# Performance work log

Hardware: AMD Instinct MI355X
Metric: run time of the kernel (lower is better)

## Reference

```python
import jax, jax.numpy as jnp
import numpy as np

B, L, D_MODEL = 2, 2048, 1024
D_STATE, D_CONV, EXPAND, DT_RANK = 16, 4, 2, 64
D_INNER = EXPAND * D_MODEL


def setup_inputs() -> dict:
    key = jax.random.key(0)
    ks = jax.random.split(key, 12)
    s = 0.02
    A_log = jnp.log(jnp.broadcast_to(jnp.arange(1, D_STATE + 1, dtype=jnp.float32), (D_INNER, D_STATE)))
    return {
        "x": jax.random.normal(ks[0], (B, L, D_MODEL), jnp.float32),
        "W_in": jax.random.normal(ks[1], (2 * D_INNER, D_MODEL), jnp.float32) * s,
        "conv_w": jax.random.normal(ks[2], (D_INNER, 1, D_CONV), jnp.float32) * 0.2,
        "conv_b": jax.random.normal(ks[3], (D_INNER,), jnp.float32) * s,
        "W_xp": jax.random.normal(ks[4], (DT_RANK + 2 * D_STATE, D_INNER), jnp.float32) * s,
        "W_dt": jax.random.normal(ks[5], (D_INNER, DT_RANK), jnp.float32) * 0.1,
        "b_dt": jax.random.uniform(ks[6], (D_INNER,), jnp.float32, -4.6, -2.3),  # ~softplus^-1 of small dt
        "A_log": A_log,
        "D": jnp.ones((D_INNER,), jnp.float32),
        "W_out_ssm": jax.random.normal(ks[7], (D_MODEL, D_INNER), jnp.float32) * s,
        "W_out": jax.random.normal(ks[8], (D_MODEL, D_MODEL), jnp.float32) * s,
        "b_out": jnp.zeros((D_MODEL,), jnp.float32),
    }


def _mamba_block(x, W_in, conv_w, conv_b, W_xp, W_dt, b_dt, A_log, D, W_out_ssm, W_out, b_out):
    d_inner = conv_b.shape[0]
    d_state = A_log.shape[1]
    dt_rank = W_dt.shape[1]
    d_conv = conv_w.shape[-1]

    # in_proj -> x branch and gate z
    xz = x @ W_in.T                         # [B, L, 2*d_inner]
    xin, z = jnp.split(xz, 2, axis=-1)

    # causal depthwise conv over time
    xc = jnp.transpose(xin, (0, 2, 1))      # [B, d_inner, L]
    xc = jax.lax.conv_general_dilated(
        xc, conv_w, window_strides=(1,), padding=[(d_conv - 1, 0)],
        feature_group_count=d_inner)
    xc = jax.nn.silu(xc + conv_b[None, :, None])
    xs = jnp.transpose(xc, (0, 2, 1))       # [B, L, d_inner]

    # input-dependent dt, B, C
    x_dbl = xs @ W_xp.T                     # [B, L, dt_rank + 2*d_state]
    dt, Bm, Cm = jnp.split(x_dbl, [dt_rank, dt_rank + d_state], axis=-1)
    dt = jax.nn.softplus(dt @ W_dt.T + b_dt)  # [B, L, d_inner]

    A = -jnp.exp(A_log)                     # [d_inner, d_state]

    def step(h, inp):
        dt_t, B_t, C_t, x_t = inp           # [B,di] [B,ds] [B,ds] [B,di]
        dA = jnp.exp(dt_t[:, :, None] * A)                      # [B, di, ds]
        h = h * dA + (dt_t * x_t)[:, :, None] * B_t[:, None, :]  # [B, di, ds]
        y = jnp.einsum('bds,bs->bd', h, C_t)
        return h, y

    h0 = jnp.zeros((x.shape[0], d_inner, d_state), x.dtype)
    tm = lambda a: jnp.swapaxes(a, 0, 1)    # time-major
    _, ys = jax.lax.scan(step, h0, (tm(dt), tm(Bm), tm(Cm), tm(xs)))
    y = jnp.swapaxes(ys, 0, 1)              # [B, L, d_inner]

    y = y + xs * D
    y = y * jax.nn.silu(z)
    y = y @ W_out_ssm.T                     # mamba-internal out_proj -> d_model
    return y @ W_out.T + b_out              # wrapper out_proj


def reference(x, W_in, conv_w, conv_b, W_xp, W_dt, b_dt, A_log, D, W_out_ssm, W_out, b_out):
    return _mamba_block(x, W_in, conv_w, conv_b, W_xp, W_dt, b_dt, A_log, D, W_out_ssm, W_out, b_out)
```

## Files before the change

### kernel.cpp

```cpp
#include <hip/hip_runtime.h>
#include <hip/hip_bf16.h>
#include <cmath>
#include <cstdint>

typedef __bf16 bf16_t;
typedef bf16_t bf16x8 __attribute__((ext_vector_type(8)));
typedef bf16_t bf16x4 __attribute__((ext_vector_type(4)));
typedef float f32x4 __attribute__((ext_vector_type(4)));

#define BB 2
#define LL 2048
#define DMODEL 1024
#define DINNER 2048
#define DSTATE 16
#define NC 64
#define CHUNK 32
#define KSEG 256

#define EXP2F(x) __builtin_amdgcn_exp2f(x)

#define CVT_N0 1048576
#define CVT_N1 2097152
#define CVT_N2 2129920
#define CVT_N3 2392064
#define CVT_NB0 9344
#define CVT_NB1 10368
#define CVT_NBT 10880
__global__ __launch_bounds__(256) void k_cvt_all(
    const float* __restrict__ x, const float* __restrict__ Win,
    const float* __restrict__ Wdt, const float* __restrict__ Wo,
    const float* __restrict__ Wxp, const float* __restrict__ Wos,
    bf16_t* __restrict__ x_b, bf16_t* __restrict__ Win_b,
    bf16_t* __restrict__ Wdt_b, bf16_t* __restrict__ Wo_b,
    bf16_t* __restrict__ Wxp_b, bf16_t* __restrict__ WosT_b) {
    const int tid = threadIdx.x;
    if (blockIdx.x < CVT_NB0) {
        int i = blockIdx.x * 256 + tid;
        const float* src; bf16_t* dst; int j;
        if (i < CVT_N0)      { src = x;   dst = x_b;   j = i; }
        else if (i < CVT_N1) { src = Win; dst = Win_b; j = i - CVT_N0; }
        else if (i < CVT_N2) { src = Wdt; dst = Wdt_b; j = i - CVT_N1; }
        else                 { src = Wo;  dst = Wo_b;  j = i - CVT_N2; }
        float4 v = reinterpret_cast<const float4*>(src)[j];
        bf16x4 o;
        o[0] = (bf16_t)v.x; o[1] = (bf16_t)v.y; o[2] = (bf16_t)v.z; o[3] = (bf16_t)v.w;
        reinterpret_cast<bf16x4*>(dst)[j] = o;
    } else if (blockIdx.x < CVT_NB1) {
        int i = (blockIdx.x - CVT_NB0) * 256 + tid;
        int r = i >> 11, c = i & (DINNER - 1);
        float v = (r < 96) ? Wxp[r * DINNER + c] : 0.f;
        Wxp_b[i] = (bf16_t)v;
    } else {
        __shared__ float tile[64][65];
        const int bid = blockIdx.x - CVT_NB1;
        const int m0 = (bid & 15) * 64;
        const int d0 = (bid >> 4) * 64;
        const int dl = tid & 63;
        #pragma unroll 4
        for (int i = 0; i < 16; ++i) {
            const int mr = (tid >> 6) + i * 4;
            tile[dl][mr] = Wos[(size_t)(m0 + mr) * DINNER + d0 + dl];
        }
        __syncthreads();
        const int dr = tid >> 2;
        const int q  = tid & 3;
        bf16_t* op = WosT_b + (size_t)(d0 + dr) * DMODEL + m0 + q * 16;
        bf16x8 v0, v1;
        #pragma unroll
        for (int j = 0; j < 8; ++j) v0[j] = (bf16_t)tile[dr][q * 16 + j];
        #pragma unroll
        for (int j = 0; j < 8; ++j) v1[j] = (bf16_t)tile[dr][q * 16 + 8 + j];
        reinterpret_cast<bf16x8*>(op)[0] = v0;
        reinterpret_cast<bf16x8*>(op)[1] = v1;
    }
}

__device__ __forceinline__ void gload16(const void* g, void* l) {
    __builtin_amdgcn_global_load_lds(
        (const __attribute__((address_space(1))) void*)g,
        (__attribute__((address_space(3))) void*)l,
        16, 0, 0);
}

__global__ __launch_bounds__(256) void k_gemm3(
    const bf16_t* __restrict__ x_b, const bf16_t* __restrict__ Win_b,
    const bf16_t* __restrict__ Wo_b, const bf16_t* __restrict__ WosT_b,
    bf16_t* __restrict__ Wc_b, bf16_t* __restrict__ xin_b,
    bf16_t* __restrict__ zsT) {
    __shared__ bf16_t sA[2][128 * 32];
    __shared__ bf16_t sB[2][128 * 32];
    const int tid = threadIdx.x;
    const int wid = tid >> 6, lane = tid & 63;

    const int bid = (blockIdx.x & 7) * 144 + (blockIdx.x >> 3);
    const bf16_t* A; const bf16_t* Bt; int N, tile, sub;
    if (bid < 128)      { sub = 0; A = Wo_b;  Bt = WosT_b; N = 2048; tile = bid; }
    else if (bid < 640) { sub = 1; A = x_b;   Bt = Win_b;  N = 2048; tile = bid - 128; }
    else                { sub = 2; A = Win_b + (size_t)DINNER * DMODEL; Bt = x_b; N = 4096; tile = bid - 640; }
    const int ntile = N >> 7;
    const int m0 = (tile / ntile) << 7;
    const int n0 = (tile % ntile) << 7;
    const int wr = wid >> 1, wc = wid & 1;
    f32x4 acc[4][4] = {};

    const bf16_t* ap = A + (size_t)(m0 + (tid >> 2)) * 1024 + (tid & 3) * 8;
    const bf16_t* bp = Bt + (size_t)(n0 + (tid >> 2)) * 1024 + (tid & 3) * 8;
    const int lm = lane & 15, lk = (lane >> 4) * 8;

    auto stage = [&](int buf, int kt) {
        char* dA = (char*)sA[buf] + wid * 1024;
        char* dB = (char*)sB[buf] + wid * 1024;
        gload16(ap + kt, dA);
        gload16(ap + kt + (size_t)64 * 1024, dA + 4096);
        gload16(bp + kt, dB);
        gload16(bp + kt + (size_t)64 * 1024, dB + 4096);
    };

    stage(0, 0);
    __syncthreads();
    int cur = 0;
    for (int kt = 0; kt < 1024; kt += 32) {
        if (kt + 32 < 1024) stage(cur ^ 1, kt + 32);
        const bf16_t* rA = sA[cur] + (wr * 64 + lm) * 32 + lk;
        const bf16_t* rB = sB[cur] + (wc * 64 + lm) * 32 + lk;
        bf16x8 fa[4], fb[4];
        #pragma unroll
        for (int i = 0; i < 4; ++i) fa[i] = *(const bf16x8*)(rA + i * 16 * 32);
        #pragma unroll
        for (int j = 0; j < 4; ++j) fb[j] = *(const bf16x8*)(rB + j * 16 * 32);
        __builtin_amdgcn_s_setprio(1);
        #pragma unroll
        for (int i = 0; i < 4; ++i)
            #pragma unroll
            for (int j = 0; j < 4; ++j)
                acc[i][j] = __builtin_amdgcn_mfma_f32_16x16x32_bf16(fa[i], fb[j], acc[i][j], 0, 0, 0);
        __builtin_amdgcn_s_setprio(0);
        __syncthreads();
        cur ^= 1;
    }

    const int row0 = m0 + wr * 64 + (lane >> 4) * 4;
    const int col0 = n0 + wc * 64 + lm;
    #pragma unroll
    for (int i = 0; i < 4; ++i) {
        #pragma unroll
        for (int j = 0; j < 4; ++j) {
            #pragma unroll
            for (int r = 0; r < 4; ++r) {
                int row = row0 + i * 16 + r;
                int c = col0 + j * 16;
                float v = acc[i][j][r];
                if (sub == 0)      Wc_b[(size_t)row * DINNER + c] = (bf16_t)v;
                else if (sub == 1) xin_b[(size_t)row * DINNER + c] = (bf16_t)v;
                else               zsT[(size_t)row * (BB * LL) + c] = (bf16_t)(v / (1.f + __expf(-v)));
            }
        }
    }
}

enum { EPI_BF16 = 0, EPI_BIAS = 1, EPI_SOFTPLUS_RB = 3, EPI_PARTK = 4 };

template <int EPI>
__global__ __launch_bounds__(512) void k_gemm_bt(
    const bf16_t* __restrict__ A, const bf16_t* __restrict__ Bt,
    int M, int N, int Kloop, int lda, int ldb,
    float* __restrict__ C, bf16_t* __restrict__ Cb,
    const float* __restrict__ bias,
    float* __restrict__ o_part) {
    __shared__ bf16_t sA[2][128 * 32];
    __shared__ bf16_t sB[2][128 * 32];
    const int tid = threadIdx.x;
    const int wid = tid >> 6, lane = tid & 63;
    const int bx = (blockIdx.x & 7) * ((int)gridDim.x >> 3) + (blockIdx.x >> 3);
    int m0, n0, k0 = 0, seg = 0;
    if (EPI == EPI_PARTK) {
        m0 = (bx & 31) << 7;
        n0 = 0;
        seg = bx >> 5;
        k0 = seg * KSEG;
    } else {
        const int ntile = N >> 7;
        m0 = (bx / ntile) << 7;
        n0 = (bx % ntile) << 7;
    }
    const int wr = wid >> 2, wc = wid & 3;
    f32x4 acc[4][2] = {};

    const bf16_t* ap = A + (size_t)(m0 + (tid >> 2)) * lda + (tid & 3) * 8 + k0;
    const bf16_t* bp = Bt + (size_t)(n0 + (tid >> 2)) * ldb + (tid & 3) * 8 + k0;
    const int lm = lane & 15, lk = (lane >> 4) * 8;

    auto stage = [&](int buf, int kt) {
        char* dA = (char*)sA[buf] + wid * 1024;
        char* dB = (char*)sB[buf] + wid * 1024;
        gload16(ap + kt, dA);
        gload16(bp + kt, dB);
    };

    stage(0, 0);
    __syncthreads();
    int cur = 0;
    for (int kt = 0; kt < Kloop; kt += 32) {
        if (kt + 32 < Kloop) stage(cur ^ 1, kt + 32);
        const bf16_t* rA = sA[cur] + (wr * 64 + lm) * 32 + lk;
        const bf16_t* rB = sB[cur] + (wc * 32 + lm) * 32 + lk;
        bf16x8 fa[4], fb[2];
        #pragma unroll
        for (int i = 0; i < 4; ++i) fa[i] = *(const bf16x8*)(rA + i * 16 * 32);
        #pragma unroll
        for (int j = 0; j < 2; ++j) fb[j] = *(const bf16x8*)(rB + j * 16 * 32);
        __builtin_amdgcn_s_setprio(1);
        #pragma unroll
        for (int i = 0; i < 4; ++i)
            #pragma unroll
            for (int j = 0; j < 2; ++j)
                acc[i][j] = __builtin_amdgcn_mfma_f32_16x16x32_bf16(fa[i], fb[j], acc[i][j], 0, 0, 0);
        __builtin_amdgcn_s_setprio(0);
        __syncthreads();
        cur ^= 1;
    }

    const int row0 = m0 + wr * 64 + (lane >> 4) * 4;
    const int col0 = n0 + wc * 32 + lm;
    float* Cp = (EPI == EPI_PARTK)
        ? o_part + (size_t)seg * ((size_t)4096 * 128)
        : C;
    #pragma unroll
    for (int i = 0; i < 4; ++i) {
        #pragma unroll
        for (int j = 0; j < 2; ++j) {
            #pragma unroll
            for (int r = 0; r < 4; ++r) {
                int row = row0 + i * 16 + r;
                int c = col0 + j * 16;
                float v = acc[i][j][r];
                if (EPI == EPI_BF16) {
                    Cb[(size_t)row * N + c] = (bf16_t)v;
                } else if (EPI == EPI_BIAS) {
                    C[(size_t)row * N + c] = v + bias[c];
                } else if (EPI == EPI_SOFTPLUS_RB) {
                    float xv = v + bias[row];
                    float sp = fmaxf(xv, 0.f) + log1pf(__expf(-fabsf(xv)));
                    Cb[(size_t)row * N + c] = (bf16_t)sp;
                } else {
                    Cp[(size_t)row * 128 + c] = v;
                }
            }
        }
    }
}

__global__ __launch_bounds__(256) void k_split_reduce(
    const float* __restrict__ part, bf16_t* __restrict__ dtr,
    float* __restrict__ Bmf, float* __restrict__ Cmf) {
    int idx = blockIdx.x * 256 + threadIdx.x;
    int row = idx >> 7, c = idx & 127;
    float s = 0.f;
    #pragma unroll
    for (int g = 0; g < 8; ++g) s += part[(size_t)g * (4096 * 128) + idx];
    if (c < 64) dtr[(size_t)row * 64 + c] = (bf16_t)s;
    else if (c < 80) Bmf[(size_t)row * 16 + (c - 64)] = s;
    else if (c < 96) Cmf[(size_t)row * 16 + (c - 80)] = s;
}

__global__ __launch_bounds__(256) void k_conv(
    const bf16_t* __restrict__ xin, const float* __restrict__ cw,
    const float* __restrict__ cb, bf16_t* __restrict__ xs_b,
    bf16_t* __restrict__ xsT) {
    __shared__ float tile[64][65];
    const int tid = threadIdx.x;
    const int d0  = (blockIdx.x & 31) * 64;
    const int bl0 = (blockIdx.x >> 5) * 64;
    const int dl = tid & 63;
    const int d  = d0 + dl;
    const float w0 = cw[d * 4], w1 = cw[d * 4 + 1], w2 = cw[d * 4 + 2], w3 = cw[d * 4 + 3];
    const float bias = cb[d];
    const int l0 = bl0 & (LL - 1);
    #pragma unroll 4
    for (int i = 0; i < 16; ++i) {
        const int blr = (tid >> 6) + i * 4;
        const int bl = bl0 + blr;
        const int l  = l0 + blr;
        const bf16_t* rp = xin + (size_t)bl * DINNER + d;
        float acc = fmaf(w3, (float)rp[0], bias);
        if (l >= 1) acc = fmaf(w2, (float)rp[-(int)DINNER], acc);
        if (l >= 2) acc = fmaf(w1, (float)rp[-2 * (int)DINNER], acc);
        if (l >= 3) acc = fmaf(w0, (float)rp[-3 * (int)DINNER], acc);
        float sv = acc / (1.f + __expf(-acc));
        xs_b[(size_t)bl * DINNER + d] = (bf16_t)sv;
        tile[dl][blr] = sv;
    }
    __syncthreads();
    const int dr = tid >> 2;
    const int q  = tid & 3;
    bf16_t* op = xsT + (size_t)(d0 + dr) * (BB * LL) + bl0 + q * 16;
    bf16x8 v0, v1;
    #pragma unroll
    for (int j = 0; j < 8; ++j) v0[j] = (bf16_t)tile[dr][q * 16 + j];
    #pragma unroll
    for (int j = 0; j < 8; ++j) v1[j] = (bf16_t)tile[dr][q * 16 + 8 + j];
    reinterpret_cast<bf16x8*>(op)[0] = v0;
    reinterpret_cast<bf16x8*>(op)[1] = v1;
}


__global__ __launch_bounds__(256) void k_scan_p1(
    const bf16_t* __restrict__ dtT, const bf16_t* __restrict__ xsT,
    const float* __restrict__ Bm, const float* __restrict__ A_log,
    float* __restrict__ alpha, float* __restrict__ beta) {
    __shared__ float sB[CHUNK * 16];
    const int db = blockIdx.x & 7;
    const int ck = (blockIdx.x >> 3) & (NC - 1);
    const int b  = blockIdx.x >> 9;
    const int tid = threadIdx.x;
    const int d  = db * 256 + tid;
    const int t0 = ck * CHUNK;

    const float* Bsrc = Bm + ((size_t)b * LL + t0) * 16;
    sB[tid] = Bsrc[tid];
    sB[tid + 256] = Bsrc[tid + 256];

    f32x4 a2[4];
    #pragma unroll
    for (int q = 0; q < 4; ++q) {
        f32x4 av = reinterpret_cast<const f32x4*>(A_log + d * 16)[q];
        #pragma unroll
        for (int j = 0; j < 4; ++j) a2[q][j] = -__expf(av[j]) * 1.44269504f;
    }
    const bf16x8* dtp = reinterpret_cast<const bf16x8*>(dtT + (size_t)d * (BB * LL) + b * LL + t0);
    const bf16x8* xsp = reinterpret_cast<const bf16x8*>(xsT + (size_t)d * (BB * LL) + b * LL + t0);

    bf16x8 dtl[4], xsl[4];
    #pragma unroll
    for (int q = 0; q < 4; ++q) dtl[q] = dtp[q];
    #pragma unroll
    for (int q = 0; q < 4; ++q) xsl[q] = xsp[q];

    __syncthreads();

    float al[16], be[16];
    #pragma unroll
    for (int s = 0; s < 16; ++s) { al[s] = 1.f; be[s] = 0.f; }

    #pragma unroll
    for (int t = 0; t < CHUNK; ++t) {
        float dtv = (float)dtl[t >> 3][t & 7];
        float xv  = (float)xsl[t >> 3][t & 7];
        float dtx = dtv * xv;
        #pragma unroll
        for (int q = 0; q < 4; ++q) {
            f32x4 Bq = *reinterpret_cast<const f32x4*>(sB + t * 16 + q * 4);
            #pragma unroll
            for (int j = 0; j < 4; ++j) {
                const int s = q * 4 + j;
                float dA = EXP2F(dtv * a2[q][j]);
                al[s] *= dA;
                be[s] = fmaf(be[s], dA, dtx * Bq[j]);
            }
        }
    }
    float* ap = alpha + ((size_t)(b * NC + ck)) * (DINNER * 16) + (size_t)d * 16;
    float* bp = beta  + ((size_t)(b * NC + ck)) * (DINNER * 16) + (size_t)d * 16;
    #pragma unroll
    for (int q = 0; q < 4; ++q) {
        f32x4 av, bv;
        #pragma unroll
        for (int j = 0; j < 4; ++j) { av[j] = al[q * 4 + j]; bv[j] = be[q * 4 + j]; }
        reinterpret_cast<f32x4*>(ap)[q] = av;
        reinterpret_cast<f32x4*>(bp)[q] = bv;
    }
}

__global__ __launch_bounds__(256) void k_scan_p2(
    const float* __restrict__ alpha, const float* __restrict__ beta,
    float* __restrict__ H) {
    const int gid = blockIdx.x * 256 + threadIdx.x;
    const int b = gid >> 15, r = gid & 32767;
    float h = 0.f;
    #pragma unroll 8
    for (int ck = 0; ck < NC; ++ck) {
        const size_t i = ((size_t)(b * NC + ck)) * 32768 + r;
        H[i] = h;
        h = fmaf(alpha[i], h, beta[i]);
    }
}

__global__ __launch_bounds__(256) void k_scan_p3(
    const bf16_t* __restrict__ dtT, const bf16_t* __restrict__ xsT,
    const float* __restrict__ Bm, const float* __restrict__ Cm,
    const bf16_t* __restrict__ zsT, const float* __restrict__ A_log,
    const float* __restrict__ Dp, const float* __restrict__ H,
    bf16_t* __restrict__ y) {
    __shared__ float sB[CHUNK * 16];
    __shared__ float sC[CHUNK * 16];
    const int db = blockIdx.x & 7;
    const int ck = (blockIdx.x >> 3) & (NC - 1);
    const int b  = blockIdx.x >> 9;
    const int tid = threadIdx.x;
    const int d  = db * 256 + tid;
    const int t0 = ck * CHUNK;

    const float* Bsrc = Bm + ((size_t)b * LL + t0) * 16;
    const float* Csrc = Cm + ((size_t)b * LL + t0) * 16;
    sB[tid] = Bsrc[tid];
    sB[tid + 256] = Bsrc[tid + 256];
    sC[tid] = Csrc[tid];
    sC[tid + 256] = Csrc[tid + 256];

    f32x4 a2[4];
    #pragma unroll
    for (int q = 0; q < 4; ++q) {
        f32x4 av = reinterpret_cast<const f32x4*>(A_log + d * 16)[q];
        #pragma unroll
        for (int j = 0; j < 4; ++j) a2[q][j] = -__expf(av[j]) * 1.44269504f;
    }
    const float Dd = Dp[d];
    const bf16x8* dtp = reinterpret_cast<const bf16x8*>(dtT + (size_t)d * (BB * LL) + b * LL + t0);
    const bf16x8* xsp = reinterpret_cast<const bf16x8*>(xsT + (size_t)d * (BB * LL) + b * LL + t0);
    const bf16x8* zp  = reinterpret_cast<const bf16x8*>(zsT + (size_t)d * (BB * LL) + b * LL + t0);
    bf16_t* yp = y + ((size_t)b * LL + t0) * DINNER + d;

    bf16x8 dtl[4], xsl[4], zsl[4];
    #pragma unroll
    for (int q = 0; q < 4; ++q) dtl[q] = dtp[q];
    #pragma unroll
    for (int q = 0; q < 4; ++q) xsl[q] = xsp[q];
    #pragma unroll
    for (int q = 0; q < 4; ++q) zsl[q] = zp[q];

    float h[16];
    {
        const f32x4* hp = reinterpret_cast<const f32x4*>(H + ((size_t)(b * NC + ck)) * 32768 + (size_t)d * 16);
        #pragma unroll
        for (int q = 0; q < 4; ++q) {
            f32x4 hv = hp[q];
            #pragma unroll
            for (int j = 0; j < 4; ++j) h[q * 4 + j] = hv[j];
        }
    }

    __syncthreads();

    #pragma unroll
    for (int t = 0; t < CHUNK; ++t) {
        float dtv = (float)dtl[t >> 3][t & 7];
        float xv  = (float)xsl[t >> 3][t & 7];
        float zv  = (float)zsl[t >> 3][t & 7];
        float dtx = dtv * xv;
        float yacc = 0.f;
        #pragma unroll
        for (int q = 0; q < 4; ++q) {
            f32x4 Bq = *reinterpret_cast<const f32x4*>(sB + t * 16 + q * 4);
            f32x4 Cq = *reinterpret_cast<const f32x4*>(sC + t * 16 + q * 4);
            #pragma unroll
            for (int j = 0; j < 4; ++j) {
                const int s = q * 4 + j;
                float dA = EXP2F(dtv * a2[q][j]);
                h[s] = fmaf(h[s], dA, dtx * Bq[j]);
                yacc = fmaf(h[s], Cq[j], yacc);
            }
        }
        float yv = (yacc + xv * Dd) * zv;
        yp[(size_t)t * DINNER] = (bf16_t)yv;
    }
}

extern "C" void kernel_launch(void* const* d_in, const int* in_sizes, int n_in,
                              void* d_out, int out_size, void* d_ws, size_t ws_size,
                              hipStream_t stream) {
    const float* x      = (const float*)d_in[0];
    const float* W_in   = (const float*)d_in[1];
    const float* conv_w = (const float*)d_in[2];
    const float* conv_b = (const float*)d_in[3];
    const float* W_xp   = (const float*)d_in[4];
    const float* W_dt   = (const float*)d_in[5];
    const float* b_dt   = (const float*)d_in[6];
    const float* A_log  = (const float*)d_in[7];
    const float* Dvec   = (const float*)d_in[8];
    const float* W_os   = (const float*)d_in[9];
    const float* W_o    = (const float*)d_in[10];
    const float* b_o    = (const float*)d_in[11];
    float* out = (float*)d_out;

    char* base = (char*)d_ws;
    size_t off = 0;
    auto alloc = [&](size_t bytes) -> char* {
        char* p = base + off;
        off += (bytes + 255) & ~(size_t)255;
        return p;
    };
    const int MR = BB * LL;
    bf16_t* x_b   = (bf16_t*)alloc((size_t)MR * DMODEL * 2);
    bf16_t* Win_b = (bf16_t*)alloc((size_t)4096 * 1024 * 2);
    bf16_t* xin_b = (bf16_t*)alloc((size_t)MR * DINNER * 2);
    bf16_t* xs_b  = (bf16_t*)alloc((size_t)MR * DINNER * 2);
    bf16_t* zsT   = (bf16_t*)alloc((size_t)DINNER * MR * 2);
    bf16_t* xsT   = (bf16_t*)alloc((size_t)DINNER * MR * 2);
    bf16_t* dtT_b = (bf16_t*)alloc((size_t)DINNER * MR * 2);
    float*  Hbuf  = (float*)alloc((size_t)BB * NC * DINNER * 16 * 4);
    bf16_t* y_b   = (bf16_t*)alloc((size_t)MR * DINNER * 2);
    bf16_t* dtr_b = (bf16_t*)alloc((size_t)MR * 64 * 2);
    float*  Bmf   = (float*)alloc((size_t)MR * 16 * 4);
    float*  Cmf   = (float*)alloc((size_t)MR * 16 * 4);
    bf16_t* Wxp_b = (bf16_t*)alloc((size_t)128 * DINNER * 2);
    bf16_t* Wdt_b = (bf16_t*)alloc((size_t)DINNER * 64 * 2);
    bf16_t* WosT_b= (bf16_t*)alloc((size_t)DINNER * DMODEL * 2);
    bf16_t* Wo_b  = (bf16_t*)alloc((size_t)DMODEL * DMODEL * 2);
    bf16_t* Wc_b  = (bf16_t*)alloc((size_t)DMODEL * DINNER * 2);

    float* alphab = (float*)xin_b;
    float* betab  = (float*)x_b;
    float* partk  = Hbuf;

    k_cvt_all<<<CVT_NBT, 256, 0, stream>>>(
        x, W_in, W_dt, W_o, W_xp, W_os,
        x_b, Win_b, Wdt_b, Wo_b, Wxp_b, WosT_b);

    k_gemm3<<<1152, 256, 0, stream>>>(
        x_b, Win_b, Wo_b, WosT_b, Wc_b, xin_b, zsT);
    k_conv<<<(MR / 64) * (DINNER / 64), 256, 0, stream>>>(xin_b, conv_w, conv_b, xs_b, xsT);
    k_gemm_bt<EPI_PARTK><<<8 * 32, 512, 0, stream>>>(
        xs_b, Wxp_b, MR, 128, KSEG, DINNER, DINNER,
        nullptr, nullptr, nullptr, partk);
    k_split_reduce<<<(MR * 128) / 256, 256, 0, stream>>>(partk, dtr_b, Bmf, Cmf);
    k_gemm_bt<EPI_SOFTPLUS_RB><<<(DINNER / 128) * (MR / 128), 512, 0, stream>>>(
        Wdt_b, dtr_b, DINNER, MR, 64, 64, 64,
        nullptr, dtT_b, b_dt, nullptr);
    k_scan_p1<<<BB * NC * (DINNER / 256), 256, 0, stream>>>(dtT_b, xsT, Bmf, A_log, alphab, betab);
    k_scan_p2<<<(BB * DINNER * DSTATE) / 256, 256, 0, stream>>>(alphab, betab, Hbuf);
    k_scan_p3<<<BB * NC * (DINNER / 256), 256, 0, stream>>>(dtT_b, xsT, Bmf, Cmf, zsT, A_log, Dvec, Hbuf, y_b);
    k_gemm_bt<EPI_BIAS><<<(MR / 128) * (DMODEL / 128), 512, 0, stream>>>(
        y_b, Wc_b, MR, DMODEL, DINNER, DINNER, DINNER,
        out, nullptr, b_o, nullptr);
}
```

Baseline: 238.2 us.

## Use 256x256 swizzled-LDS tiles for in_proj GEMM and split weight-combine GEMM

The fused three-way 128x128 GEMM kernel is replaced by a dedicated 512-thread kernel with 256x256 output tiles. It uses a K-step of 64, XOR-swizzled LDS layout and double-buffered direct global-to-LDS loads, computing the x and gate projections in 256 blocks. The Wo·Wos weight-combine product moves to a separate launch of the generic GEMM kernel. The larger tiles are meant to raise data reuse per LDS load and cut global traffic, at the cost of 128 KB LDS per block, one extra kernel launch, and a single wave of large blocks.

```diff
diff --git a/kernel.cpp b/kernel.cpp
--- a/kernel.cpp
+++ b/kernel.cpp
@@ -82,77 +82,102 @@
         16, 0, 0);
 }
 
-__global__ __launch_bounds__(256) void k_gemm3(
+__global__ __launch_bounds__(512) void k_gemm256(
     const bf16_t* __restrict__ x_b, const bf16_t* __restrict__ Win_b,
-    const bf16_t* __restrict__ Wo_b, const bf16_t* __restrict__ WosT_b,
-    bf16_t* __restrict__ Wc_b, bf16_t* __restrict__ xin_b,
-    bf16_t* __restrict__ zsT) {
-    __shared__ bf16_t sA[2][128 * 32];
-    __shared__ bf16_t sB[2][128 * 32];
+    bf16_t* __restrict__ xin_b, bf16_t* __restrict__ zsT) {
+    __shared__ bf16_t lds[65536];
     const int tid = threadIdx.x;
     const int wid = tid >> 6, lane = tid & 63;
 
-    const int bid = (blockIdx.x & 7) * 144 + (blockIdx.x >> 3);
-    const bf16_t* A; const bf16_t* Bt; int N, tile, sub;
-    if (bid < 128)      { sub = 0; A = Wo_b;  Bt = WosT_b; N = 2048; tile = bid; }
-    else if (bid < 640) { sub = 1; A = x_b;   Bt = Win_b;  N = 2048; tile = bid - 128; }
-    else                { sub = 2; A = Win_b + (size_t)DINNER * DMODEL; Bt = x_b; N = 4096; tile = bid - 640; }
-    const int ntile = N >> 7;
-    const int m0 = (tile / ntile) << 7;
-    const int n0 = (tile % ntile) << 7;
-    const int wr = wid >> 1, wc = wid & 1;
-    f32x4 acc[4][4] = {};
-
-    const bf16_t* ap = A + (size_t)(m0 + (tid >> 2)) * 1024 + (tid & 3) * 8;
-    const bf16_t* bp = Bt + (size_t)(n0 + (tid >> 2)) * 1024 + (tid & 3) * 8;
-    const int lm = lane & 15, lk = (lane >> 4) * 8;
-
-    auto stage = [&](int buf, int kt) {
-        char* dA = (char*)sA[buf] + wid * 1024;
-        char* dB = (char*)sB[buf] + wid * 1024;
-        gload16(ap + kt, dA);
-        gload16(ap + kt + (size_t)64 * 1024, dA + 4096);
-        gload16(bp + kt, dB);
-        gload16(bp + kt + (size_t)64 * 1024, dB + 4096);
+    const int bid = (blockIdx.x & 7) * 32 + (blockIdx.x >> 3);
+    const bf16_t* A; const bf16_t* Bt; int m0, n0, sub;
+    if (bid < 128) {
+        sub = 0; A = x_b; Bt = Win_b;
+        m0 = (bid >> 3) * 256; n0 = (bid & 7) * 256;
+    } else {
+        sub = 1; A = Win_b + (size_t)DINNER * DMODEL; Bt = x_b;
+        const int t2 = bid - 128;
+        m0 = (t2 >> 4) * 256; n0 = (t2 & 15) * 256;
+    }
+    const int wr = wid >> 2, wc = wid & 3;
+    f32x4 acc[8][4] = {};
+
+    const int srow = tid >> 3;
+    const int k8p = (tid & 7) ^ (srow & 7);
+    const bf16_t* apA = A + (size_t)(m0 + srow) * 1024 + k8p * 8;
+    const bf16_t* apB = Bt + (size_t)(n0 + srow) * 1024 + k8p * 8;
+
+    auto stageA = [&](int slot, int kt) {
+        char* b0 = (char*)lds + slot * 32768 + wid * 1024;
+        const bf16_t* src = apA + kt * 64;
+        gload16(src, b0);
+        gload16(src + (size_t)64 * 1024, b0 + 8192);
+        gload16(src + (size_t)128 * 1024, b0 + 16384);
+        gload16(src + (size_t)192 * 1024, b0 + 24576);
     };
-
-    stage(0, 0);
-    __syncthreads();
-    int cur = 0;
-    for (int kt = 0; kt < 1024; kt += 32) {
-        if (kt + 32 < 1024) stage(cur ^ 1, kt + 32);
-        const bf16_t* rA = sA[cur] + (wr * 64 + lm) * 32 + lk;
-        const bf16_t* rB = sB[cur] + (wc * 64 + lm) * 32 + lk;
-        bf16x8 fa[4], fb[4];
-        #pragma unroll
-        for (int i = 0; i < 4; ++i) fa[i] = *(const bf16x8*)(rA + i * 16 * 32);
-        #pragma unroll
-        for (int j = 0; j < 4; ++j) fb[j] = *(const bf16x8*)(rB + j * 16 * 32);
-        __builtin_amdgcn_s_setprio(1);
-        #pragma unroll
-        for (int i = 0; i < 4; ++i)
-            #pragma unroll
-            for (int j = 0; j < 4; ++j)
-                acc[i][j] = __builtin_amdgcn_mfma_f32_16x16x32_bf16(fa[i], fb[j], acc[i][j], 0, 0, 0);
-        __builtin_amdgcn_s_setprio(0);
-        __syncthreads();
-        cur ^= 1;
-    }
-
-    const int row0 = m0 + wr * 64 + (lane >> 4) * 4;
+    auto stageB = [&](int slot, int kt) {
+        char* b0 = (char*)lds + 65536 + slot * 32768 + wid * 1024;
+        const bf16_t* src = apB + kt * 64;
+        gload16(src, b0);
+        gload16(src + (size_t)64 * 1024, b0 + 8192);
+        gload16(src + (size_t)128 * 1024, b0 + 16384);
+        gload16(src + (size_t)192 * 1024, b0 + 24576);
+    };
+
+    const int lm = lane & 15, lq = lane >> 4;
+
+    stageA(0, 0);
+    stageB(0, 0);
+    for (int t = 0; t < 16; ++t) {
+        const int s = t & 1;
+        asm volatile("s_waitcnt vmcnt(0)" ::: "memory");
+        __builtin_amdgcn_sched_barrier(0);
+        __builtin_amdgcn_s_barrier();
+        __builtin_amdgcn_sched_barrier(0);
+        if (t + 1 < 16) stageA(s ^ 1, t + 1);
+
+        const bf16_t* Ab = lds + s * 16384 + wr * 8192;
+        const bf16_t* Bb = lds + 32768 + s * 16384 + (wc >> 1) * 8192;
+        const int brr0 = (wc & 1) * 64;
+        #pragma unroll
+        for (int ks = 0; ks < 2; ++ks) {
+            if (ks == 1 && t + 1 < 16) stageB(s ^ 1, t + 1);
+            bf16x8 fa[8], fb[4];
+            #pragma unroll
+            for (int i = 0; i < 8; ++i) {
+                const int rr = lm + i * 16;
+                const int sl = ((lq + 4 * ks) ^ (rr & 7));
+                fa[i] = *(const bf16x8*)(Ab + rr * 64 + sl * 8);
+            }
+            #pragma unroll
+            for (int j = 0; j < 4; ++j) {
+                const int rr = brr0 + lm + j * 16;
+                const int sl = ((lq + 4 * ks) ^ (rr & 7));
+                fb[j] = *(const bf16x8*)(Bb + rr * 64 + sl * 8);
+            }
+            __builtin_amdgcn_s_setprio(1);
+            #pragma unroll
+            for (int i = 0; i < 8; ++i)
+                #pragma unroll
+                for (int j = 0; j < 4; ++j)
+                    acc[i][j] = __builtin_amdgcn_mfma_f32_16x16x32_bf16(fa[i], fb[j], acc[i][j], 0, 0, 0);
+            __builtin_amdgcn_s_setprio(0);
+        }
+    }
+
+    const int row0 = m0 + wr * 128 + lq * 4;
     const int col0 = n0 + wc * 64 + lm;
     #pragma unroll
-    for (int i = 0; i < 4; ++i) {
+    for (int i = 0; i < 8; ++i) {
         #pragma unroll
         for (int j = 0; j < 4; ++j) {
             #pragma unroll
             for (int r = 0; r < 4; ++r) {
-                int row = row0 + i * 16 + r;
-                int c = col0 + j * 16;
+                const int row = row0 + i * 16 + r;
+                const int c = col0 + j * 16;
                 float v = acc[i][j][r];
-                if (sub == 0)      Wc_b[(size_t)row * DINNER + c] = (bf16_t)v;
-                else if (sub == 1) xin_b[(size_t)row * DINNER + c] = (bf16_t)v;
-                else               zsT[(size_t)row * (BB * LL) + c] = (bf16_t)(v / (1.f + __expf(-v)));
+                if (sub == 0) xin_b[(size_t)row * DINNER + c] = (bf16_t)v;
+                else          zsT[(size_t)row * (BB * LL) + c] = (bf16_t)(v / (1.f + __expf(-v)));
             }
         }
     }
@@ -516,8 +541,10 @@
         x, W_in, W_dt, W_o, W_xp, W_os,
         x_b, Win_b, Wdt_b, Wo_b, Wxp_b, WosT_b);
 
-    k_gemm3<<<1152, 256, 0, stream>>>(
-        x_b, Win_b, Wo_b, WosT_b, Wc_b, xin_b, zsT);
+    k_gemm_bt<EPI_BF16><<<(DMODEL / 128) * (DINNER / 128), 512, 0, stream>>>(
+        Wo_b, WosT_b, DMODEL, DINNER, DMODEL, DMODEL, DMODEL,
+        nullptr, Wc_b, nullptr, nullptr);
+    k_gemm256<<<256, 512, 0, stream>>>(x_b, Win_b, xin_b, zsT);
     k_conv<<<(MR / 64) * (DINNER / 64), 256, 0, stream>>>(xin_b, conv_w, conv_b, xs_b, xsT);
     k_gemm_bt<EPI_PARTK><<<8 * 32, 512, 0, stream>>>(
         xs_b, Wxp_b, MR, 128, KSEG, DINNER, DINNER,
```

Result: no change. 242.4 us (+1.8%).
